# Optimization experiments

Measured on AMD Instinct MI355X. Metric: run time of the kernel, lower is better.

The kernel has to match this reference:

```python
import jax, jax.numpy as jnp
import numpy as np

B = 131072   # batched ODE states
D = 32       # state dim (net1 in/out)
H1 = 50      # net1 hidden
Q = 528      # tril(outer(y,y)) feature count = D*(D+1)//2
H2 = 700     # net2 hidden

# static lower-triangular index pairs for the quadratic feature expansion
_ROWS, _COLS = np.tril_indices(D)
_ROWS = jnp.asarray(_ROWS)
_COLS = jnp.asarray(_COLS)


def setup_inputs() -> dict:
    key = jax.random.key(0)
    ks = jax.random.split(key, 6)
    y = jax.random.normal(ks[0], (B, D), dtype=jnp.float32)
    t = jnp.zeros((1,), dtype=jnp.float32)  # unused by the dynamics
    # weights init: normal(0, 0.1), biases zero (as in the torch module)
    W1a = 0.1 * jax.random.normal(ks[1], (D, H1), dtype=jnp.float32)
    b1a = jnp.zeros((H1,), dtype=jnp.float32)
    W1b = 0.1 * jax.random.normal(ks[2], (H1, D), dtype=jnp.float32)
    b1b = jnp.zeros((D,), dtype=jnp.float32)
    W2a = 0.1 * jax.random.normal(ks[3], (Q, H2), dtype=jnp.float32)
    b2a = jnp.zeros((H2,), dtype=jnp.float32)
    W2b = 0.1 * jax.random.normal(ks[4], (H2, D), dtype=jnp.float32)
    b2b = jnp.zeros((D,), dtype=jnp.float32)
    return dict(t=t, y=y, W1a=W1a, b1a=b1a, W1b=W1b, b1b=b1b,
                W2a=W2a, b2a=b2a, W2b=W2b, b2b=b2b)


def reference(t, y, W1a, b1a, W1b, b1b, W2a, b2a, W2b, b2b):
    # quadratic_y: lower triangle of outer(y, y), vectorized over batch
    quad = y[:, _ROWS] * y[:, _COLS]               # [B, 528]
    out1 = jnp.tanh(y @ W1a + b1a) @ W1b + b1b     # [B, 32]
    out2 = jnp.tanh(quad @ W2a + b2a) @ W2b + b2b  # [B, 32]
    return out1 + out2
```

## Files before the change

kernel.cpp:

```cpp
#include <hip/hip_runtime.h>
#include <hip/hip_bf16.h>

#define B_TOT 131072
#define D     32
#define H1    50
#define QF    528
#define H2    700
#define MROWS 64
#define QSTR  584
#define KITER 18

typedef __attribute__((ext_vector_type(8))) short  short8x;
typedef __attribute__((ext_vector_type(4))) float  floatx4;

static __device__ __forceinline__ unsigned short f2bf(float f) {
    __hip_bfloat16 h = __float2bfloat16(f);
    return __builtin_bit_cast(unsigned short, h);
}
static __device__ __forceinline__ float bf2f(unsigned short u) {
    unsigned int x = (unsigned int)u << 16;
    return __builtin_bit_cast(float, x);
}
static __device__ __forceinline__ float tanh_fast(float x) {
    float e = __builtin_amdgcn_exp2f(x * 2.885390082f);
    return 1.f - 2.f * __builtin_amdgcn_rcpf(e + 1.f);
}

__global__ void prep_kernel(const float* __restrict__ W2a, const float* __restrict__ b2a,
                            const float* __restrict__ W2b,
                            const float* __restrict__ W1a, const float* __restrict__ b1a,
                            const float* __restrict__ W1b, const float* __restrict__ b1b,
                            const float* __restrict__ b2b,
                            unsigned short* __restrict__ W2aT,
                            unsigned short* __restrict__ W2bT) {
    int idx = blockIdx.x * 256 + threadIdx.x;
    const int N1 = KITER * 48 * 512;
    const int N2 = 16 * 4 * 512;
    if (idx < N1) {
        int k   = idx / (48 * 512);
        int rem = idx - k * (48 * 512);
        int p   = rem >> 9;
        int q   = rem & 511;
        int ln  = q >> 3, j = q & 7;
        int kk  = k * 32 + ((ln >> 4) << 3) + j;
        int c   = (p << 4) + (ln & 15);
        float v = 0.f;
        if (c < H2) {
            if (kk < QF)       v = W2a[kk * H2 + c];
            else if (kk == QF) v = b2a[c];
        } else if (c < H2 + H1) {
            int cc = c - H2;
            if (kk == QF)                        v = b1a[cc];
            else if (kk > QF && kk < QF + 1 + D) v = W1a[(kk - QF - 1) * H1 + cc];
        } else if (c == H2 + H1) {
            if (kk == QF) v = 1.0f;
        }
        W2aT[idx] = f2bf(v);
    } else if (idx < N1 + N2) {
        int i2 = idx - N1;
        int q  = i2 & 511;
        int ln = q >> 3, j = q & 7;
        int w  = i2 >> 11;
        int ks = (i2 >> 10) & 1;
        int of = (i2 >> 9) & 1;
        int kl = (ks << 5) + ((ln >> 4) << 3) + j;
        int kg = w * 48 + kl;
        int c  = (of << 4) + (ln & 15);
        float v = 0.f;
        if (kl < 48) {
            if (kg < H2)            v = W2b[kg * D + c];
            else if (kg < H2 + H1)  v = W1b[(kg - H2) * D + c];
            else if (kg == H2 + H1) v = (b1b[c] + b2b[c]) / tanh_fast(1.0f);
        }
        W2bT[i2] = f2bf(v);
    }
}

__global__ __launch_bounds__(1024)
__attribute__((amdgpu_waves_per_eu(4, 4)))
void fused_kernel(
    const float* __restrict__ y,
    const unsigned short* __restrict__ W2aT, const unsigned short* __restrict__ W2bT,
    float* __restrict__ out) {

    __shared__ unsigned short quadls[MROWS][QSTR];
    __shared__ float          yls[MROWS][36];
    __shared__ unsigned short hst[16][16][68];

    const int tid  = threadIdx.x;
    const int lane = tid & 63;
    const int w    = tid >> 6;
    const int wu   = __builtin_amdgcn_readfirstlane(w);
    const int l15  = lane & 15;
    const int lg   = lane >> 4;
    const int row0 = blockIdx.x * MROWS;
    unsigned short* stage = &quadls[0][0];

    yls[tid >> 5][tid & 31] = y[row0 * D + tid];
    yls[32 + (tid >> 5)][tid & 31] = y[row0 * D + 1024 + tid];
    {
        int rr = lane >> 2, cc0 = 48 + (lane & 3) * 4;
        *reinterpret_cast<unsigned long long*>(&hst[w][rr][cc0]) = 0ULL;
    }
    __syncthreads();

    #pragma unroll
    for (int s = 0; s < 2; ++s) {
        int task = tid + s * 1024;
        int r = task >> 5, i = task & 31;
        int base = (i * (i + 1)) >> 1;
        float yi = yls[r][i];
        for (int j4 = 0; j4 <= i; j4 += 4) {
            floatx4 yv = *reinterpret_cast<const floatx4*>(&yls[r][j4]);
            #pragma unroll
            for (int jj = 0; jj < 4; ++jj) {
                int j = j4 + jj;
                if (j <= i) quadls[r][base + j] = f2bf(yi * yv[jj]);
            }
        }
        quadls[r][529 + i] = f2bf(yi);
        if (i == 0)  quadls[r][528] = (unsigned short)0x3F80;
        if (i < 15)  quadls[r][561 + i] = 0;
    }
    __syncthreads();

    floatx4 hacc[4][3];
    #pragma unroll
    for (int m = 0; m < 4; ++m)
        #pragma unroll
        for (int nf = 0; nf < 3; ++nf) hacc[m][nf] = (floatx4){0.f, 0.f, 0.f, 0.f};
    {
        const unsigned short* bp = W2aT + wu * 3 * 512 + lane * 8;
        #pragma unroll 2
        for (int k = 0; k < KITER; ++k) {
            short8x a[4];
            #pragma unroll
            for (int m = 0; m < 4; ++m)
                a[m] = *reinterpret_cast<const short8x*>(&quadls[m * 16 + l15][k * 32 + lg * 8]);
            short8x b0 = *reinterpret_cast<const short8x*>(bp);
            short8x b1 = *reinterpret_cast<const short8x*>(bp + 512);
            short8x b2 = *reinterpret_cast<const short8x*>(bp + 1024);
            #pragma unroll
            for (int m = 0; m < 4; ++m) {
                hacc[m][0] = __builtin_amdgcn_mfma_f32_16x16x32_bf16(a[m], b0, hacc[m][0], 0, 0, 0);
                hacc[m][1] = __builtin_amdgcn_mfma_f32_16x16x32_bf16(a[m], b1, hacc[m][1], 0, 0, 0);
                hacc[m][2] = __builtin_amdgcn_mfma_f32_16x16x32_bf16(a[m], b2, hacc[m][2], 0, 0, 0);
            }
            bp += 48 * 512;
        }
    }
    __syncthreads();

    {
        const unsigned short* wb = W2bT + wu * 4 * 512 + lane * 8;
        #pragma unroll
        for (int m = 0; m < 4; ++m) {
            #pragma unroll
            for (int r = 0; r < 4; ++r) {
                hst[w][lg * 4 + r][l15]      = f2bf(tanh_fast(hacc[m][0][r]));
                hst[w][lg * 4 + r][16 + l15] = f2bf(tanh_fast(hacc[m][1][r]));
                hst[w][lg * 4 + r][32 + l15] = f2bf(tanh_fast(hacc[m][2][r]));
            }
            short8x aa0 = *reinterpret_cast<const short8x*>(&hst[w][l15][lg * 8]);
            short8x aa1 = *reinterpret_cast<const short8x*>(&hst[w][l15][32 + lg * 8]);
            floatx4 o20 = {0,0,0,0}, o21 = {0,0,0,0};
            {
                short8x bw00 = *reinterpret_cast<const short8x*>(wb);
                short8x bw01 = *reinterpret_cast<const short8x*>(wb + 512);
                o20 = __builtin_amdgcn_mfma_f32_16x16x32_bf16(aa0, bw00, o20, 0, 0, 0);
                o21 = __builtin_amdgcn_mfma_f32_16x16x32_bf16(aa0, bw01, o21, 0, 0, 0);
            }
            {
                short8x bw10 = *reinterpret_cast<const short8x*>(wb + 1024);
                short8x bw11 = *reinterpret_cast<const short8x*>(wb + 1536);
                o20 = __builtin_amdgcn_mfma_f32_16x16x32_bf16(aa1, bw10, o20, 0, 0, 0);
                o21 = __builtin_amdgcn_mfma_f32_16x16x32_bf16(aa1, bw11, o21, 0, 0, 0);
            }
            #pragma unroll
            for (int r = 0; r < 4; ++r) {
                int row = m * 16 + lg * 4 + r;
                unsigned int pk = ((unsigned int)f2bf(o21[r]) << 16) | (unsigned int)f2bf(o20[r]);
                *reinterpret_cast<unsigned int*>(&stage[wu * 2048 + row * 32 + l15 * 2]) = pk;
            }
        }
    }
    __syncthreads();

    {
        #pragma unroll
        for (int s = 0; s < 2; ++s) {
            int e  = tid + s * 1024;
            int c  = e & 31;
            int fr = (e & ~31) + ((c & 15) << 1) + (c >> 4);
            float s0 = 0.f, s1 = 0.f;
            #pragma unroll
            for (int p = 0; p < 16; p += 2) {
                s0 += bf2f(stage[p * 2048 + fr]);
                s1 += bf2f(stage[(p + 1) * 2048 + fr]);
            }
            out[row0 * D + e] = s0 + s1;
        }
    }
}

extern "C" void kernel_launch(void* const* d_in, const int* in_sizes, int n_in,
                              void* d_out, int out_size, void* d_ws, size_t ws_size,
                              hipStream_t stream) {
    const float* y   = (const float*)d_in[1];
    const float* W1a = (const float*)d_in[2];
    const float* b1a = (const float*)d_in[3];
    const float* W1b = (const float*)d_in[4];
    const float* b1b = (const float*)d_in[5];
    const float* W2a = (const float*)d_in[6];
    const float* b2a = (const float*)d_in[7];
    const float* W2b = (const float*)d_in[8];
    const float* b2b = (const float*)d_in[9];

    unsigned short* W2aT = (unsigned short*)d_ws;
    unsigned short* W2bT = (unsigned short*)((char*)d_ws + 884736);

    const int prep_tasks = KITER * 48 * 512 + 16 * 4 * 512;
    prep_kernel<<<(prep_tasks + 255) / 256, 256, 0, stream>>>(
        W2a, b2a, W2b, W1a, b1a, W1b, b1b, b2b, W2aT, W2bT);
    fused_kernel<<<B_TOT / MROWS, 1024, 0, stream>>>(y, W2aT, W2bT, (float*)d_out);
}
```

Baseline: 152.1 us.

## Switch to 32x32x16 MFMA tiles with 8 waves per block

Replaces the 16x16x32 bf16 MFMA tiling with 32x32x16 MFMAs. Each of 8 waves now owns 96 hidden columns, where before each of 16 waves owned 48. The packed weight layouts are repacked to match. Larger MFMA tiles cut LDS A-operand reads per flop, and halving the waves halves the cross-wave partial-sum reduction. The cost is lower occupancy (2 waves/EU) and more accumulator registers per wave.

```diff
diff --git a/kernel.cpp b/kernel.cpp
--- a/kernel.cpp
+++ b/kernel.cpp
@@ -8,10 +8,13 @@
 #define H2    700
 #define MROWS 64
 #define QSTR  584
-#define KITER 18
-
-typedef __attribute__((ext_vector_type(8))) short  short8x;
-typedef __attribute__((ext_vector_type(4))) float  floatx4;
+#define KSTEPS 36
+#define NTILE  24
+
+typedef __attribute__((ext_vector_type(8)))  short  short8x;
+typedef __attribute__((ext_vector_type(4)))  float  floatx4;
+typedef __attribute__((ext_vector_type(16))) float  floatx16;
+typedef __attribute__((ext_vector_type(4)))  unsigned short ushort4x;
 
 static __device__ __forceinline__ unsigned short f2bf(float f) {
     __hip_bfloat16 h = __float2bfloat16(f);
@@ -34,16 +37,16 @@
                             unsigned short* __restrict__ W2aT,
                             unsigned short* __restrict__ W2bT) {
     int idx = blockIdx.x * 256 + threadIdx.x;
-    const int N1 = KITER * 48 * 512;
-    const int N2 = 16 * 4 * 512;
+    const int N1 = KSTEPS * NTILE * 512;
+    const int N2 = 8 * 6 * 512;
     if (idx < N1) {
-        int k   = idx / (48 * 512);
-        int rem = idx - k * (48 * 512);
-        int p   = rem >> 9;
+        int ks  = idx / (NTILE * 512);
+        int rem = idx - ks * (NTILE * 512);
+        int t   = rem >> 9;
         int q   = rem & 511;
         int ln  = q >> 3, j = q & 7;
-        int kk  = k * 32 + ((ln >> 4) << 3) + j;
-        int c   = (p << 4) + (ln & 15);
+        int kk  = ks * 16 + ((ln >> 5) << 3) + j;
+        int c   = (t << 5) + (ln & 31);
         float v = 0.f;
         if (c < H2) {
             if (kk < QF)       v = W2a[kk * H2 + c];
@@ -58,26 +61,23 @@
         W2aT[idx] = f2bf(v);
     } else if (idx < N1 + N2) {
         int i2 = idx - N1;
-        int q  = i2 & 511;
+        int w  = i2 / (6 * 512);
+        int rem = i2 - w * (6 * 512);
+        int s  = rem >> 9;
+        int q  = rem & 511;
         int ln = q >> 3, j = q & 7;
-        int w  = i2 >> 11;
-        int ks = (i2 >> 10) & 1;
-        int of = (i2 >> 9) & 1;
-        int kl = (ks << 5) + ((ln >> 4) << 3) + j;
-        int kg = w * 48 + kl;
-        int c  = (of << 4) + (ln & 15);
+        int kg = w * 96 + s * 16 + ((ln >> 5) << 3) + j;
+        int c  = ln & 31;
         float v = 0.f;
-        if (kl < 48) {
-            if (kg < H2)            v = W2b[kg * D + c];
-            else if (kg < H2 + H1)  v = W1b[(kg - H2) * D + c];
-            else if (kg == H2 + H1) v = (b1b[c] + b2b[c]) / tanh_fast(1.0f);
-        }
+        if (kg < H2)            v = W2b[kg * D + c];
+        else if (kg < H2 + H1)  v = W1b[(kg - H2) * D + c];
+        else if (kg == H2 + H1) v = (b1b[c] + b2b[c]) / tanh_fast(1.0f);
         W2bT[i2] = f2bf(v);
     }
 }
 
-__global__ __launch_bounds__(1024)
-__attribute__((amdgpu_waves_per_eu(4, 4)))
+__global__ __launch_bounds__(512)
+__attribute__((amdgpu_waves_per_eu(2, 2)))
 void fused_kernel(
     const float* __restrict__ y,
     const unsigned short* __restrict__ W2aT, const unsigned short* __restrict__ W2bT,
@@ -85,28 +85,27 @@
 
     __shared__ unsigned short quadls[MROWS][QSTR];
     __shared__ float          yls[MROWS][36];
-    __shared__ unsigned short hst[16][16][68];
+    __shared__ unsigned short hst[8][32][104];
 
     const int tid  = threadIdx.x;
     const int lane = tid & 63;
     const int w    = tid >> 6;
     const int wu   = __builtin_amdgcn_readfirstlane(w);
-    const int l15  = lane & 15;
-    const int lg   = lane >> 4;
+    const int l31  = lane & 31;
+    const int h    = lane >> 5;
     const int row0 = blockIdx.x * MROWS;
-    unsigned short* stage = &quadls[0][0];
-
-    yls[tid >> 5][tid & 31] = y[row0 * D + tid];
-    yls[32 + (tid >> 5)][tid & 31] = y[row0 * D + 1024 + tid];
-    {
-        int rr = lane >> 2, cc0 = 48 + (lane & 3) * 4;
-        *reinterpret_cast<unsigned long long*>(&hst[w][rr][cc0]) = 0ULL;
+    unsigned short* panel = &quadls[0][0];
+
+    {
+        int r = tid >> 3, c = (tid & 7) * 4;
+        floatx4 v = *reinterpret_cast<const floatx4*>(y + (row0 + r) * D + c);
+        *reinterpret_cast<floatx4*>(&yls[r][c]) = v;
     }
     __syncthreads();
 
     #pragma unroll
-    for (int s = 0; s < 2; ++s) {
-        int task = tid + s * 1024;
+    for (int s = 0; s < 4; ++s) {
+        int task = tid + s * 512;
         int r = task >> 5, i = task & 31;
         int base = (i * (i + 1)) >> 1;
         float yi = yls[r][i];
@@ -124,82 +123,80 @@
     }
     __syncthreads();
 
-    floatx4 hacc[4][3];
+    floatx16 acc[2][3];
     #pragma unroll
-    for (int m = 0; m < 4; ++m)
-        #pragma unroll
-        for (int nf = 0; nf < 3; ++nf) hacc[m][nf] = (floatx4){0.f, 0.f, 0.f, 0.f};
+    for (int m = 0; m < 2; ++m)
+        #pragma unroll
+        for (int t = 0; t < 3; ++t)
+            acc[m][t] = (floatx16)(0.f);
     {
         const unsigned short* bp = W2aT + wu * 3 * 512 + lane * 8;
         #pragma unroll 2
-        for (int k = 0; k < KITER; ++k) {
-            short8x a[4];
-            #pragma unroll
-            for (int m = 0; m < 4; ++m)
-                a[m] = *reinterpret_cast<const short8x*>(&quadls[m * 16 + l15][k * 32 + lg * 8]);
+        for (int ks = 0; ks < KSTEPS; ++ks) {
+            short8x a0 = *reinterpret_cast<const short8x*>(&quadls[l31][ks * 16 + h * 8]);
+            short8x a1 = *reinterpret_cast<const short8x*>(&quadls[32 + l31][ks * 16 + h * 8]);
             short8x b0 = *reinterpret_cast<const short8x*>(bp);
             short8x b1 = *reinterpret_cast<const short8x*>(bp + 512);
             short8x b2 = *reinterpret_cast<const short8x*>(bp + 1024);
-            #pragma unroll
-            for (int m = 0; m < 4; ++m) {
-                hacc[m][0] = __builtin_amdgcn_mfma_f32_16x16x32_bf16(a[m], b0, hacc[m][0], 0, 0, 0);
-                hacc[m][1] = __builtin_amdgcn_mfma_f32_16x16x32_bf16(a[m], b1, hacc[m][1], 0, 0, 0);
-                hacc[m][2] = __builtin_amdgcn_mfma_f32_16x16x32_bf16(a[m], b2, hacc[m][2], 0, 0, 0);
+            acc[0][0] = __builtin_amdgcn_mfma_f32_32x32x16_bf16(a0, b0, acc[0][0], 0, 0, 0);
+            acc[0][1] = __builtin_amdgcn_mfma_f32_32x32x16_bf16(a0, b1, acc[0][1], 0, 0, 0);
+            acc[0][2] = __builtin_amdgcn_mfma_f32_32x32x16_bf16(a0, b2, acc[0][2], 0, 0, 0);
+            acc[1][0] = __builtin_amdgcn_mfma_f32_32x32x16_bf16(a1, b0, acc[1][0], 0, 0, 0);
+            acc[1][1] = __builtin_amdgcn_mfma_f32_32x32x16_bf16(a1, b1, acc[1][1], 0, 0, 0);
+            acc[1][2] = __builtin_amdgcn_mfma_f32_32x32x16_bf16(a1, b2, acc[1][2], 0, 0, 0);
+            bp += NTILE * 512;
+        }
+    }
+    __syncthreads();
+
+    {
+        const unsigned short* wb = W2bT + wu * 6 * 512 + lane * 8;
+        short8x bw[6];
+        #pragma unroll
+        for (int s = 0; s < 6; ++s)
+            bw[s] = *reinterpret_cast<const short8x*>(wb + s * 512);
+
+        #pragma unroll
+        for (int m = 0; m < 2; ++m) {
+            #pragma unroll
+            for (int t = 0; t < 3; ++t)
+                #pragma unroll
+                for (int reg = 0; reg < 16; ++reg)
+                    hst[w][(reg & 3) + 8 * (reg >> 2) + 4 * h][t * 32 + l31]
+                        = f2bf(tanh_fast(acc[m][t][reg]));
+            floatx16 o2 = (floatx16)(0.f);
+            #pragma unroll
+            for (int s = 0; s < 6; ++s) {
+                short8x a2 = *reinterpret_cast<const short8x*>(&hst[w][l31][s * 16 + h * 8]);
+                o2 = __builtin_amdgcn_mfma_f32_32x32x16_bf16(a2, bw[s], o2, 0, 0, 0);
             }
-            bp += 48 * 512;
-        }
-    }
-    __syncthreads();
-
-    {
-        const unsigned short* wb = W2bT + wu * 4 * 512 + lane * 8;
-        #pragma unroll
-        for (int m = 0; m < 4; ++m) {
-            #pragma unroll
-            for (int r = 0; r < 4; ++r) {
-                hst[w][lg * 4 + r][l15]      = f2bf(tanh_fast(hacc[m][0][r]));
-                hst[w][lg * 4 + r][16 + l15] = f2bf(tanh_fast(hacc[m][1][r]));
-                hst[w][lg * 4 + r][32 + l15] = f2bf(tanh_fast(hacc[m][2][r]));
+            #pragma unroll
+            for (int q = 0; q < 4; ++q) {
+                ushort4x pk;
+                #pragma unroll
+                for (int i = 0; i < 4; ++i)
+                    pk[i] = f2bf(o2[4 * q + i]);
+                *reinterpret_cast<ushort4x*>(
+                    &panel[wu * 2176 + l31 * 68 + m * 32 + 8 * q + 4 * h]) = pk;
             }
-            short8x aa0 = *reinterpret_cast<const short8x*>(&hst[w][l15][lg * 8]);
-            short8x aa1 = *reinterpret_cast<const short8x*>(&hst[w][l15][32 + lg * 8]);
-            floatx4 o20 = {0,0,0,0}, o21 = {0,0,0,0};
-            {
-                short8x bw00 = *reinterpret_cast<const short8x*>(wb);
-                short8x bw01 = *reinterpret_cast<const short8x*>(wb + 512);
-                o20 = __builtin_amdgcn_mfma_f32_16x16x32_bf16(aa0, bw00, o20, 0, 0, 0);
-                o21 = __builtin_amdgcn_mfma_f32_16x16x32_bf16(aa0, bw01, o21, 0, 0, 0);
-            }
-            {
-                short8x bw10 = *reinterpret_cast<const short8x*>(wb + 1024);
-                short8x bw11 = *reinterpret_cast<const short8x*>(wb + 1536);
-                o20 = __builtin_amdgcn_mfma_f32_16x16x32_bf16(aa1, bw10, o20, 0, 0, 0);
-                o21 = __builtin_amdgcn_mfma_f32_16x16x32_bf16(aa1, bw11, o21, 0, 0, 0);
-            }
-            #pragma unroll
-            for (int r = 0; r < 4; ++r) {
-                int row = m * 16 + lg * 4 + r;
-                unsigned int pk = ((unsigned int)f2bf(o21[r]) << 16) | (unsigned int)f2bf(o20[r]);
-                *reinterpret_cast<unsigned int*>(&stage[wu * 2048 + row * 32 + l15 * 2]) = pk;
-            }
-        }
-    }
-    __syncthreads();
-
-    {
-        #pragma unroll
-        for (int s = 0; s < 2; ++s) {
-            int e  = tid + s * 1024;
-            int c  = e & 31;
-            int fr = (e & ~31) + ((c & 15) << 1) + (c >> 4);
-            float s0 = 0.f, s1 = 0.f;
-            #pragma unroll
-            for (int p = 0; p < 16; p += 2) {
-                s0 += bf2f(stage[p * 2048 + fr]);
-                s1 += bf2f(stage[(p + 1) * 2048 + fr]);
-            }
-            out[row0 * D + e] = s0 + s1;
-        }
+        }
+    }
+    __syncthreads();
+
+    {
+        int c  = tid & 31;
+        int rg = tid >> 5;
+        int base = c * 68 + rg * 4;
+        float s0 = 0.f, s1 = 0.f, s2 = 0.f, s3 = 0.f;
+        #pragma unroll
+        for (int p = 0; p < 8; ++p) {
+            ushort4x v = *reinterpret_cast<const ushort4x*>(&panel[p * 2176 + base]);
+            s0 += bf2f(v[0]); s1 += bf2f(v[1]); s2 += bf2f(v[2]); s3 += bf2f(v[3]);
+        }
+        out[(row0 + rg * 4 + 0) * D + c] = s0;
+        out[(row0 + rg * 4 + 1) * D + c] = s1;
+        out[(row0 + rg * 4 + 2) * D + c] = s2;
+        out[(row0 + rg * 4 + 3) * D + c] = s3;
     }
 }
 
@@ -219,8 +216,8 @@
     unsigned short* W2aT = (unsigned short*)d_ws;
     unsigned short* W2bT = (unsigned short*)((char*)d_ws + 884736);
 
-    const int prep_tasks = KITER * 48 * 512 + 16 * 4 * 512;
+    const int prep_tasks = KSTEPS * NTILE * 512 + 8 * 6 * 512;
     prep_kernel<<<(prep_tasks + 255) / 256, 256, 0, stream>>>(
         W2a, b2a, W2b, W1a, b1a, W1b, b1b, b2b, W2aT, W2bT);
-    fused_kernel<<<B_TOT / MROWS, 1024, 0, stream>>>(y, W2aT, W2bT, (float*)d_out);
-}
+    fused_kernel<<<B_TOT / MROWS, 512, 0, stream>>>(y, W2aT, W2bT, (float*)d_out);
+}
```

Measured after the change: 178.2 us. +17.2%, slower.
